# Optimization experiments

Hardware: AMD Instinct MI355X
Metric: run time of the kernel (lower is better)

Reference implementation:

```python
import jax, jax.numpy as jnp
import numpy as np

# dims: B batch, R seq_num (MSA rows), L seq_len (residues), D emb_dim, C n_emb_2D, H heads
B, R, L, D, C, H = 1, 256, 384, 512, 256, 4
HD = D // H
SCALE = np.float32((HD ** -0.5) / np.sqrt(L))  # head-dim scaling * seqlen_scaling (1/sqrt(L))
EPS = 1e-5


def setup_inputs() -> dict:
    key = jax.random.key(0)
    ks = jax.random.split(key, 6)
    s = 0.02
    return {
        "x": jax.random.normal(ks[0], (B, R, L, D), jnp.float32),
        "pair_feat": jax.random.normal(ks[1], (B, L, L, C), jnp.float32),
        "attn_mask": jnp.ones((B, L), jnp.int32),
        "ln_msa_g": jnp.ones((D,), jnp.float32),
        "ln_msa_b": jnp.zeros((D,), jnp.float32),
        "ln_pair_g": jnp.ones((C,), jnp.float32),
        "ln_pair_b": jnp.zeros((C,), jnp.float32),
        "W_pair": jax.random.normal(ks[2], (C, H), jnp.float32) * s,  # stacked per-head [C,1] linears
        "W_v": jax.random.normal(ks[3], (D, D), jnp.float32) * s,     # stacked per-head [D,HD] value proj
        "W_out": jax.random.normal(ks[4], (D, D), jnp.float32) * s,   # to_out (bias=False)
    }


def _ln(x, g, b):
    mu = jnp.mean(x, axis=-1, keepdims=True)
    var = jnp.mean(jnp.square(x - mu), axis=-1, keepdims=True)
    return (x - mu) * jax.lax.rsqrt(var + EPS) * g + b


def reference(x, pair_feat, attn_mask, ln_msa_g, ln_msa_b, ln_pair_g, ln_pair_b, W_pair, W_v, W_out):
    # MHPair_to_MSA.forward (eval mode, dropout=0)
    msa = _ln(x, ln_msa_g, ln_msa_b)                                  # [B,R,L,D]
    pf = (pair_feat + jnp.swapaxes(pair_feat, 1, 2)) * 0.5            # symmetrize
    pf = _ln(pf, ln_pair_g, ln_pair_b)                                # [B,L,L,C]
    # pair-feature-derived attention logits (no QK^T)
    logits = jnp.einsum('bijc,ch->bhij', pf * SCALE, W_pair)          # [B,H,L,L]
    V = jnp.einsum('brld,de->brle', msa, W_v).reshape(B, R, L, H, HD) # [B,R,L,H,HD]
    mask2 = attn_mask[:, :, None] * attn_mask[:, None, :]             # [B,L,L]
    logits = jnp.where(mask2[:, None, :, :] == 0,
                       jnp.finfo(logits.dtype).min, logits)
    attn = jax.nn.softmax(logits, axis=-1)                            # [B,H,L,L]
    out = jnp.einsum('bhij,brjhd->brihd', attn, V).reshape(B, R, L, D)
    out = out @ W_out                                                 # to_out, bias=False
    return x + out                                                    # residual
```

## Files before the change

kernel.cpp:

```cpp
#include <hip/hip_runtime.h>

#define L_   384
#define D_   512
#define C_   256
#define H_   4
#define RR_  256
#define M1_  98304
#define LL2_ 147456
#define NPAIR_BLOCKS 18480

typedef __bf16 bf16x8 __attribute__((ext_vector_type(8)));
typedef float f32x4 __attribute__((ext_vector_type(4)));

__device__ __forceinline__ unsigned short f2bf_bits(float f) {
  union { float f; unsigned u; } v; v.f = f;
  return (unsigned short)((v.u + 0x7fffu + ((v.u >> 16) & 1u)) >> 16);
}
__device__ __forceinline__ __bf16 f2bf(float f) {
  union { unsigned short s; __bf16 b; } o; o.s = f2bf_bits(f);
  return o.b;
}

__global__ __launch_bounds__(256) void ln_msa_kernel(
    const float* __restrict__ x, const float* __restrict__ g,
    const float* __restrict__ b, __bf16* __restrict__ msa) {
  int row = blockIdx.x * 4 + (threadIdx.x >> 6);
  int lane = threadIdx.x & 63;
  const float4* xr = (const float4*)(x + (size_t)row * D_ + lane * 8);
  float4 v0 = xr[0], v1 = xr[1];
  float s1 = v0.x + v0.y + v0.z + v0.w + v1.x + v1.y + v1.z + v1.w;
  float s2 = v0.x * v0.x + v0.y * v0.y + v0.z * v0.z + v0.w * v0.w +
             v1.x * v1.x + v1.y * v1.y + v1.z * v1.z + v1.w * v1.w;
#pragma unroll
  for (int o = 32; o > 0; o >>= 1) {
    s1 += __shfl_xor(s1, o);
    s2 += __shfl_xor(s2, o);
  }
  float mu = s1 * (1.0f / D_);
  float var = s2 * (1.0f / D_) - mu * mu;
  float rs = rsqrtf(var + 1e-5f);
  const float4* gp = (const float4*)(g + lane * 8);
  const float4* bp = (const float4*)(b + lane * 8);
  float4 g0 = gp[0], g1 = gp[1], b0 = bp[0], b1 = bp[1];
  float y[8];
  y[0] = (v0.x - mu) * rs * g0.x + b0.x;
  y[1] = (v0.y - mu) * rs * g0.y + b0.y;
  y[2] = (v0.z - mu) * rs * g0.z + b0.z;
  y[3] = (v0.w - mu) * rs * g0.w + b0.w;
  y[4] = (v1.x - mu) * rs * g1.x + b1.x;
  y[5] = (v1.y - mu) * rs * g1.y + b1.y;
  y[6] = (v1.z - mu) * rs * g1.z + b1.z;
  y[7] = (v1.w - mu) * rs * g1.w + b1.w;
  uint4 pk;
  pk.x = ((unsigned)f2bf_bits(y[1]) << 16) | f2bf_bits(y[0]);
  pk.y = ((unsigned)f2bf_bits(y[3]) << 16) | f2bf_bits(y[2]);
  pk.z = ((unsigned)f2bf_bits(y[5]) << 16) | f2bf_bits(y[4]);
  pk.w = ((unsigned)f2bf_bits(y[7]) << 16) | f2bf_bits(y[6]);
  *(uint4*)(msa + (size_t)row * D_ + lane * 8) = pk;
}

__global__ __launch_bounds__(256) void pair_logits_kernel(
    const float* __restrict__ pf, const int* __restrict__ mask,
    const float* __restrict__ g, const float* __restrict__ b,
    const float* __restrict__ Wp, float* __restrict__ logits) {
  unsigned wid = blockIdx.x * 4 + (threadIdx.x >> 6);
  int lane = threadIdx.x & 63;
  unsigned a = wid / 385u;
  unsigned c = wid - a * 385u;
  int i, j;
  if (c < 384u - a) { i = a; j = a + c; }
  else { i = 383 - a; j = i + (c - (384 - a)); }

  int c0 = lane * 4;
  float4 p1 = *(const float4*)(pf + ((size_t)i * L_ + j) * C_ + c0);
  float4 p2 = *(const float4*)(pf + ((size_t)j * L_ + i) * C_ + c0);
  float4 v;
  v.x = 0.5f * (p1.x + p2.x); v.y = 0.5f * (p1.y + p2.y);
  v.z = 0.5f * (p1.z + p2.z); v.w = 0.5f * (p1.w + p2.w);
  float s1 = v.x + v.y + v.z + v.w;
  float s2 = v.x * v.x + v.y * v.y + v.z * v.z + v.w * v.w;
#pragma unroll
  for (int o = 32; o > 0; o >>= 1) {
    s1 += __shfl_xor(s1, o);
    s2 += __shfl_xor(s2, o);
  }
  float mu = s1 * (1.0f / C_);
  float var = s2 * (1.0f / C_) - mu * mu;
  float rs = rsqrtf(var + 1e-5f);
  float4 gv = *(const float4*)(g + c0);
  float4 bv = *(const float4*)(b + c0);
  float y0 = (v.x - mu) * rs * gv.x + bv.x;
  float y1 = (v.y - mu) * rs * gv.y + bv.y;
  float y2 = (v.z - mu) * rs * gv.z + bv.z;
  float y3 = (v.w - mu) * rs * gv.w + bv.w;
  const float4* wp = (const float4*)Wp;
  float4 w0 = wp[c0], w1 = wp[c0 + 1], w2 = wp[c0 + 2], w3 = wp[c0 + 3];
  float4 t;
  t.x = y0 * w0.x + y1 * w1.x + y2 * w2.x + y3 * w3.x;
  t.y = y0 * w0.y + y1 * w1.y + y2 * w2.y + y3 * w3.y;
  t.z = y0 * w0.z + y1 * w1.z + y2 * w2.z + y3 * w3.z;
  t.w = y0 * w0.w + y1 * w1.w + y2 * w2.w + y3 * w3.w;
#pragma unroll
  for (int o = 32; o > 0; o >>= 1) {
    t.x += __shfl_xor(t.x, o);
    t.y += __shfl_xor(t.y, o);
    t.z += __shfl_xor(t.z, o);
    t.w += __shfl_xor(t.w, o);
  }
  if (lane < 8) {
    int h = lane & 3;
    int ii = (lane < 4) ? i : j;
    int jj = (lane < 4) ? j : i;
    bool ok = (mask[i] != 0) && (mask[j] != 0);
    const float NEG = -3.402823466e38f;
    const float SCALE = (float)(0.08838834764831845 / 19.595917942265423);
    float th = (h == 0) ? t.x : (h == 1) ? t.y : (h == 2) ? t.z : t.w;
    logits[(size_t)h * LL2_ + (size_t)ii * L_ + jj] = ok ? SCALE * th : NEG;
  }
}

__global__ __launch_bounds__(256) void softmax_kernel(
    const float* __restrict__ logits, __bf16* __restrict__ attn) {
  int wave = threadIdx.x >> 6, lane = threadIdx.x & 63;
  int row = blockIdx.x * 4 + wave;
  const float* lr = logits + (size_t)row * L_;
  float v[6];
#pragma unroll
  for (int t = 0; t < 6; ++t) v[t] = lr[lane + t * 64];
  float mx = v[0];
#pragma unroll
  for (int t = 1; t < 6; ++t) mx = fmaxf(mx, v[t]);
#pragma unroll
  for (int o = 32; o > 0; o >>= 1) mx = fmaxf(mx, __shfl_xor(mx, o));
  float s = 0.f;
#pragma unroll
  for (int t = 0; t < 6; ++t) { v[t] = __expf(v[t] - mx); s += v[t]; }
#pragma unroll
  for (int o = 32; o > 0; o >>= 1) s += __shfl_xor(s, o);
  float inv = 1.0f / s;
  __bf16* ar = attn + (size_t)row * L_;
#pragma unroll
  for (int t = 0; t < 6; ++t) ar[lane + t * 64] = f2bf(v[t] * inv);
}

__global__ __launch_bounds__(256) void wtrans_kernel(
    const float* __restrict__ Wv, const float* __restrict__ Wo,
    __bf16* __restrict__ WvT, __bf16* __restrict__ WoT) {
  int id = blockIdx.x * 256 + threadIdx.x;
  int m = id >> 18;
  int e = (id >> 9) & 511, d = id & 511;
  const float* W = m ? Wo : Wv;
  __bf16* T = m ? WoT : WvT;
  T[(size_t)e * 512 + d] = f2bf(W[(size_t)d * 512 + e]);
}

__device__ __forceinline__ void gload16(const void* g, void* l) {
  __builtin_amdgcn_global_load_lds(
      (const __attribute__((address_space(1))) void*)g,
      (__attribute__((address_space(3))) void*)l, 16, 0, 0);
}

__device__ __forceinline__ unsigned xcd_swz_3072(unsigned bid) {
  return (bid & 7u) * 384u + (bid >> 3);
}
__device__ __forceinline__ unsigned xcd_swz_768(unsigned bid) {
  return (bid & 7u) * 96u + (bid >> 3);
}

template <int NT>
__device__ __forceinline__ void stage_part32(__bf16* s, const __bf16* g, size_t ld) {
  int tid = threadIdx.x;
#pragma unroll
  for (int i = 0; i < 2; ++i) {
    int cid = i * NT + tid;
    int row = cid >> 2, c = cid & 3;
    int cs = c ^ ((row >> 1) & 3);
    gload16(g + (size_t)row * ld + cs * 8, (char*)s + cid * 16);
  }
}

__device__ __forceinline__ bf16x8 frag_ld32(const __bf16* s, int row, int fk) {
  int c = (fk >> 3) ^ ((row >> 1) & 3);
  return *(const bf16x8*)((const char*)s + row * 64 + c * 16);
}

__device__ __forceinline__ void mainloop256_2s(
    const __bf16* __restrict__ A, size_t ldA,
    const __bf16* __restrict__ B, size_t ldB,
    int K, __bf16* lds, f32x4 acc[8][4]) {
  int lane = threadIdx.x & 63, wave = threadIdx.x >> 6;
  int wm = (wave >> 2) * 128, wn = (wave & 3) * 64;
  int fr = lane & 15, fk = (lane >> 4) * 8;
  int nt = K >> 5;
  const int SLOT = 512 * 32;
  stage_part32<512>(lds, A, ldA);
  stage_part32<512>(lds + 256 * 32, B, ldB);
  for (int t = 0; t < nt; ++t) {
    const __bf16* As = lds + (t & 1) * SLOT;
    const __bf16* Bs = As + 256 * 32;
    if (t + 1 < nt) {
      __bf16* d = lds + ((t + 1) & 1) * SLOT;
      stage_part32<512>(d, A + (size_t)(t + 1) * 32, ldA);
      stage_part32<512>(d + 256 * 32, B + (size_t)(t + 1) * 32, ldB);
      asm volatile("s_waitcnt vmcnt(4)" ::: "memory");
    } else {
      asm volatile("s_waitcnt vmcnt(0)" ::: "memory");
    }
    __builtin_amdgcn_s_barrier();
    bf16x8 bfv[4];
#pragma unroll
    for (int ni = 0; ni < 4; ++ni) bfv[ni] = frag_ld32(Bs, wn + ni * 16 + fr, fk);
#pragma unroll
    for (int half = 0; half < 2; ++half) {
      bf16x8 af[4];
#pragma unroll
      for (int mi = 0; mi < 4; ++mi)
        af[mi] = frag_ld32(As, wm + half * 64 + mi * 16 + fr, fk);
      __builtin_amdgcn_s_setprio(1);
#pragma unroll
      for (int mi = 0; mi < 4; ++mi)
#pragma unroll
        for (int ni = 0; ni < 4; ++ni)
          acc[half * 4 + mi][ni] = __builtin_amdgcn_mfma_f32_16x16x32_bf16(
              af[mi], bfv[ni], acc[half * 4 + mi][ni], 0, 0, 0);
      __builtin_amdgcn_s_setprio(0);
    }
  }
}

__device__ __forceinline__ void mainloop128(
    const __bf16* __restrict__ A, size_t ldA,
    const __bf16* __restrict__ B, size_t ldB,
    int K, __bf16* lds, f32x4 acc[4][4]) {
  int lane = threadIdx.x & 63, wave = threadIdx.x >> 6;
  int wm = (wave >> 1) * 64, wn = (wave & 1) * 64;
  int fr = lane & 15, fk = (lane >> 4) * 8;
  int nt = K >> 5;
  const int SLOT = 256 * 32;
#pragma unroll
  for (int t = 0; t < 3; ++t) {
    stage_part32<256>(lds + t * SLOT, A + t * 32, ldA);
    stage_part32<256>(lds + t * SLOT + 128 * 32, B + t * 32, ldB);
  }
  for (int t = 0; t < nt; ++t) {
    int rem = nt - 1 - t;
    if (rem >= 2)      asm volatile("s_waitcnt vmcnt(8)" ::: "memory");
    else if (rem == 1) asm volatile("s_waitcnt vmcnt(4)" ::: "memory");
    else               asm volatile("s_waitcnt vmcnt(0)" ::: "memory");
    __builtin_amdgcn_s_barrier();
    const __bf16* As = lds + (t & 3) * SLOT;
    const __bf16* Bs = As + 128 * 32;
    if (t + 3 < nt) {
      __bf16* d = lds + ((t + 3) & 3) * SLOT;
      stage_part32<256>(d, A + (size_t)(t + 3) * 32, ldA);
      stage_part32<256>(d + 128 * 32, B + (size_t)(t + 3) * 32, ldB);
    }
    bf16x8 bfv[4];
#pragma unroll
    for (int ni = 0; ni < 4; ++ni) bfv[ni] = frag_ld32(Bs, wn + ni * 16 + fr, fk);
#pragma unroll
    for (int half = 0; half < 2; ++half) {
      bf16x8 af[2];
#pragma unroll
      for (int mi = 0; mi < 2; ++mi)
        af[mi] = frag_ld32(As, wm + half * 32 + mi * 16 + fr, fk);
      __builtin_amdgcn_s_setprio(1);
#pragma unroll
      for (int mi = 0; mi < 2; ++mi)
#pragma unroll
        for (int ni = 0; ni < 4; ++ni)
          acc[half * 2 + mi][ni] = __builtin_amdgcn_mfma_f32_16x16x32_bf16(
              af[mi], bfv[ni], acc[half * 2 + mi][ni], 0, 0, 0);
      __builtin_amdgcn_s_setprio(0);
    }
  }
}

__global__ __launch_bounds__(512) void gemm_vt_kernel(
    const __bf16* __restrict__ WvT, const __bf16* __restrict__ msa,
    __bf16* __restrict__ VT) {
  __shared__ __bf16 lds[2 * 512 * 32];
  unsigned swz = xcd_swz_768(blockIdx.x + 2 * blockIdx.y);
  int m0 = (swz & 1) * 256;
  int n0 = (swz >> 1) * 256;
  f32x4 acc[8][4] = {};
  mainloop256_2s(WvT + (size_t)m0 * D_, D_, msa + (size_t)n0 * D_, D_, D_, lds, acc);
  int lane = threadIdx.x & 63, wave = threadIdx.x >> 6;
  int wn = (wave & 3) * 64;
  int cr = (lane >> 4) * 4, cc = lane & 15;
  __bf16* Ep = lds;

  __syncthreads();
#pragma unroll
  for (int p = 0; p < 4; ++p) {
    if ((wave >> 2) == (p >> 1)) {
      int mi0 = (p & 1) * 4;
#pragma unroll
      for (int mi = 0; mi < 4; ++mi)
#pragma unroll
        for (int ni = 0; ni < 4; ++ni)
#pragma unroll
          for (int rr = 0; rr < 4; ++rr) {
            int rowl = mi * 16 + cr + rr;
            int col = wn + ni * 16 + cc;
            int cch = col >> 3;
            Ep[rowl * 256 + (((cch ^ (rowl & 31)) << 3) | (col & 7))] =
                f2bf(acc[mi0 + mi][ni][rr]);
          }
    }
    __syncthreads();
#pragma unroll
    for (int s = 0; s < 4; ++s) {
      int rowl = wave * 8 + s * 2 + (lane >> 5);
      int cch = lane & 31;
      bf16x8 v = *(const bf16x8*)&Ep[rowl * 256 + ((cch ^ (rowl & 31)) << 3)];
      int e = m0 + p * 64 + rowl;
      *(bf16x8*)(VT + (size_t)e * M1_ + n0 + cch * 8) = v;
    }
    __syncthreads();
  }
}

__global__ __launch_bounds__(256) void attnv_kernel(
    const __bf16* __restrict__ attn, const __bf16* __restrict__ VT,
    __bf16* __restrict__ out2) {
  __shared__ __bf16 lds[4 * 256 * 32];
  unsigned swz = xcd_swz_3072(blockIdx.x + 3 * blockIdx.y);
  int it = swz % 3u;
  int rh = swz / 3u;
  int h = rh & 3, r = rh >> 2;
  const __bf16* A = attn + (size_t)h * LL2_ + (size_t)it * 128 * L_;
  const __bf16* Bt = VT + (size_t)(h * 128) * M1_ + (size_t)r * L_;
  f32x4 acc[4][4] = {};
  mainloop128(A, L_, Bt, M1_, L_, lds, acc);
  int lane = threadIdx.x & 63, wave = threadIdx.x >> 6;
  int wm = (wave >> 1) * 64, wn = (wave & 1) * 64;
  int cr = (lane >> 4) * 4, cc = lane & 15;
  __bf16* Ep = lds;

  __syncthreads();
#pragma unroll
  for (int mi = 0; mi < 4; ++mi)
#pragma unroll
    for (int ni = 0; ni < 4; ++ni)
#pragma unroll
      for (int rr = 0; rr < 4; ++rr) {
        int il = wm + mi * 16 + cr + rr;
        int el = wn + ni * 16 + cc;
        int cch = el >> 3;
        Ep[il * 128 + (((cch ^ (il & 15)) << 3) | (el & 7))] =
            f2bf(acc[mi][ni][rr]);
      }
  __syncthreads();
#pragma unroll
  for (int s = 0; s < 8; ++s) {
    int il = wave * 32 + s * 4 + (lane >> 4);
    int cch = lane & 15;
    bf16x8 v = *(const bf16x8*)&Ep[il * 128 + ((cch ^ (il & 15)) << 3)];
    *(bf16x8*)(out2 + ((size_t)(r * L_ + it * 128 + il)) * D_ + h * 128 + cch * 8) = v;
  }
}

__global__ __launch_bounds__(512) void gemm_out_kernel(
    const __bf16* __restrict__ out2, const __bf16* __restrict__ WoT,
    const float* __restrict__ x, float* __restrict__ out) {
  __shared__ __bf16 lds[2 * 512 * 32];
  unsigned swz = xcd_swz_768(blockIdx.x + 2 * blockIdx.y);
  int n0 = (swz & 1) * 256;
  int m0 = (swz >> 1) * 256;
  f32x4 acc[8][4] = {};
  mainloop256_2s(out2 + (size_t)m0 * D_, D_, WoT + (size_t)n0 * D_, D_, D_, lds, acc);
  int lane = threadIdx.x & 63, wave = threadIdx.x >> 6;
  int wn = (wave & 3) * 64;
  int cr = (lane >> 4) * 4, cc = lane & 15;
  float* Ep = (float*)lds;

  __syncthreads();
#pragma unroll
  for (int p = 0; p < 4; ++p) {
    if ((wave >> 2) == (p >> 1)) {
      int mi0 = (p & 1) * 4;
#pragma unroll
      for (int mi = 0; mi < 4; ++mi)
#pragma unroll
        for (int ni = 0; ni < 4; ++ni)
#pragma unroll
          for (int rr = 0; rr < 4; ++rr) {
            int rowl = mi * 16 + cr + rr;
            int col = wn + ni * 16 + cc;
            int c4 = col >> 2;
            Ep[rowl * 256 + (((c4 ^ (rowl & 15)) << 2) | (col & 3))] =
                acc[mi0 + mi][ni][rr];
          }
    }
    __syncthreads();
#pragma unroll
    for (int s = 0; s < 8; ++s) {
      int rowl = wave * 8 + s;
      int grow = m0 + p * 64 + rowl;
      float4 v = *(float4*)&Ep[rowl * 256 + ((lane ^ (rowl & 15)) << 2)];
      float4 xv = *(const float4*)(x + (size_t)grow * D_ + n0 + lane * 4);
      v.x += xv.x; v.y += xv.y; v.z += xv.z; v.w += xv.w;
      *(float4*)(out + (size_t)grow * D_ + n0 + lane * 4) = v;
    }
    __syncthreads();
  }
}

extern "C" void kernel_launch(void* const* d_in, const int* in_sizes, int n_in,
                              void* d_out, int out_size, void* d_ws, size_t ws_size,
                              hipStream_t stream) {
  const float* x      = (const float*)d_in[0];
  const float* pair   = (const float*)d_in[1];
  const int*   mask   = (const int*)d_in[2];
  const float* g_msa  = (const float*)d_in[3];
  const float* b_msa  = (const float*)d_in[4];
  const float* g_pair = (const float*)d_in[5];
  const float* b_pair = (const float*)d_in[6];
  const float* Wp     = (const float*)d_in[7];
  const float* Wv     = (const float*)d_in[8];
  const float* Wo     = (const float*)d_in[9];
  float* out = (float*)d_out;

  char* p = (char*)d_ws;
  auto alloc = [&](size_t bytes) {
    char* r = p;
    p += (bytes + 255) & ~(size_t)255;
    return r;
  };
  __bf16* msa    = (__bf16*)alloc((size_t)M1_ * D_ * 2);
  __bf16* VT     = (__bf16*)alloc((size_t)D_ * M1_ * 2);
  float*  logits = (float*)alloc((size_t)H_ * LL2_ * 4);
  __bf16* attn   = (__bf16*)alloc((size_t)H_ * LL2_ * 2);
  __bf16* WvT    = (__bf16*)alloc((size_t)512 * 512 * 2);
  __bf16* WoT    = (__bf16*)alloc((size_t)512 * 512 * 2);
  __bf16* out2   = msa;

  wtrans_kernel<<<2048, 256, 0, stream>>>(Wv, Wo, WvT, WoT);
  ln_msa_kernel<<<M1_ / 4, 256, 0, stream>>>(x, g_msa, b_msa, msa);
  gemm_vt_kernel<<<dim3(2, M1_ / 256), 512, 0, stream>>>(WvT, msa, VT);
  pair_logits_kernel<<<NPAIR_BLOCKS, 256, 0, stream>>>(pair, mask, g_pair, b_pair, Wp, logits);
  softmax_kernel<<<(H_ * L_) / 4, 256, 0, stream>>>(logits, attn);
  attnv_kernel<<<dim3(3, RR_ * H_), 256, 0, stream>>>(attn, VT, out2);
  gemm_out_kernel<<<dim3(2, M1_ / 256), 512, 0, stream>>>(out2, WoT, x, out);
}
```

Measured before the change: 362.9 us.

## Fuse independent kernels into two heterogeneous launches

Merges the LayerNorm of the MSA with the weight transpose into one launch, and the value-projection GEMM with the pair-logit computation into another, dispatching on block index. This removes two kernel launches and lets the memory-bound pair-feature pass overlap with the compute-bound GEMM. Pair blocks now use 512 threads and inherit the GEMM's static shared memory allocation, which may lower their occupancy.

After: 390.6 us. 1.08x slower.

```diff
diff --git a/kernel.cpp b/kernel.cpp
--- a/kernel.cpp
+++ b/kernel.cpp
@@ -7,7 +7,9 @@
 #define RR_  256
 #define M1_  98304
 #define LL2_ 147456
-#define NPAIR_BLOCKS 18480
+#define NVT_BLOCKS 768
+#define NPAIR_FAT 9240
+#define NLN_BLOCKS 24576
 
 typedef __bf16 bf16x8 __attribute__((ext_vector_type(8)));
 typedef float f32x4 __attribute__((ext_vector_type(4)));
@@ -21,101 +23,52 @@
   return o.b;
 }
 
-__global__ __launch_bounds__(256) void ln_msa_kernel(
+__global__ __launch_bounds__(256) void ln_wtrans_kernel(
     const float* __restrict__ x, const float* __restrict__ g,
-    const float* __restrict__ b, __bf16* __restrict__ msa) {
-  int row = blockIdx.x * 4 + (threadIdx.x >> 6);
-  int lane = threadIdx.x & 63;
-  const float4* xr = (const float4*)(x + (size_t)row * D_ + lane * 8);
-  float4 v0 = xr[0], v1 = xr[1];
-  float s1 = v0.x + v0.y + v0.z + v0.w + v1.x + v1.y + v1.z + v1.w;
-  float s2 = v0.x * v0.x + v0.y * v0.y + v0.z * v0.z + v0.w * v0.w +
-             v1.x * v1.x + v1.y * v1.y + v1.z * v1.z + v1.w * v1.w;
-#pragma unroll
-  for (int o = 32; o > 0; o >>= 1) {
-    s1 += __shfl_xor(s1, o);
-    s2 += __shfl_xor(s2, o);
-  }
-  float mu = s1 * (1.0f / D_);
-  float var = s2 * (1.0f / D_) - mu * mu;
-  float rs = rsqrtf(var + 1e-5f);
-  const float4* gp = (const float4*)(g + lane * 8);
-  const float4* bp = (const float4*)(b + lane * 8);
-  float4 g0 = gp[0], g1 = gp[1], b0 = bp[0], b1 = bp[1];
-  float y[8];
-  y[0] = (v0.x - mu) * rs * g0.x + b0.x;
-  y[1] = (v0.y - mu) * rs * g0.y + b0.y;
-  y[2] = (v0.z - mu) * rs * g0.z + b0.z;
-  y[3] = (v0.w - mu) * rs * g0.w + b0.w;
-  y[4] = (v1.x - mu) * rs * g1.x + b1.x;
-  y[5] = (v1.y - mu) * rs * g1.y + b1.y;
-  y[6] = (v1.z - mu) * rs * g1.z + b1.z;
-  y[7] = (v1.w - mu) * rs * g1.w + b1.w;
-  uint4 pk;
-  pk.x = ((unsigned)f2bf_bits(y[1]) << 16) | f2bf_bits(y[0]);
-  pk.y = ((unsigned)f2bf_bits(y[3]) << 16) | f2bf_bits(y[2]);
-  pk.z = ((unsigned)f2bf_bits(y[5]) << 16) | f2bf_bits(y[4]);
-  pk.w = ((unsigned)f2bf_bits(y[7]) << 16) | f2bf_bits(y[6]);
-  *(uint4*)(msa + (size_t)row * D_ + lane * 8) = pk;
-}
-
-__global__ __launch_bounds__(256) void pair_logits_kernel(
-    const float* __restrict__ pf, const int* __restrict__ mask,
-    const float* __restrict__ g, const float* __restrict__ b,
-    const float* __restrict__ Wp, float* __restrict__ logits) {
-  unsigned wid = blockIdx.x * 4 + (threadIdx.x >> 6);
-  int lane = threadIdx.x & 63;
-  unsigned a = wid / 385u;
-  unsigned c = wid - a * 385u;
-  int i, j;
-  if (c < 384u - a) { i = a; j = a + c; }
-  else { i = 383 - a; j = i + (c - (384 - a)); }
-
-  int c0 = lane * 4;
-  float4 p1 = *(const float4*)(pf + ((size_t)i * L_ + j) * C_ + c0);
-  float4 p2 = *(const float4*)(pf + ((size_t)j * L_ + i) * C_ + c0);
-  float4 v;
-  v.x = 0.5f * (p1.x + p2.x); v.y = 0.5f * (p1.y + p2.y);
-  v.z = 0.5f * (p1.z + p2.z); v.w = 0.5f * (p1.w + p2.w);
-  float s1 = v.x + v.y + v.z + v.w;
-  float s2 = v.x * v.x + v.y * v.y + v.z * v.z + v.w * v.w;
-#pragma unroll
-  for (int o = 32; o > 0; o >>= 1) {
-    s1 += __shfl_xor(s1, o);
-    s2 += __shfl_xor(s2, o);
-  }
-  float mu = s1 * (1.0f / C_);
-  float var = s2 * (1.0f / C_) - mu * mu;
-  float rs = rsqrtf(var + 1e-5f);
-  float4 gv = *(const float4*)(g + c0);
-  float4 bv = *(const float4*)(b + c0);
-  float y0 = (v.x - mu) * rs * gv.x + bv.x;
-  float y1 = (v.y - mu) * rs * gv.y + bv.y;
-  float y2 = (v.z - mu) * rs * gv.z + bv.z;
-  float y3 = (v.w - mu) * rs * gv.w + bv.w;
-  const float4* wp = (const float4*)Wp;
-  float4 w0 = wp[c0], w1 = wp[c0 + 1], w2 = wp[c0 + 2], w3 = wp[c0 + 3];
-  float4 t;
-  t.x = y0 * w0.x + y1 * w1.x + y2 * w2.x + y3 * w3.x;
-  t.y = y0 * w0.y + y1 * w1.y + y2 * w2.y + y3 * w3.y;
-  t.z = y0 * w0.z + y1 * w1.z + y2 * w2.z + y3 * w3.z;
-  t.w = y0 * w0.w + y1 * w1.w + y2 * w2.w + y3 * w3.w;
-#pragma unroll
-  for (int o = 32; o > 0; o >>= 1) {
-    t.x += __shfl_xor(t.x, o);
-    t.y += __shfl_xor(t.y, o);
-    t.z += __shfl_xor(t.z, o);
-    t.w += __shfl_xor(t.w, o);
-  }
-  if (lane < 8) {
-    int h = lane & 3;
-    int ii = (lane < 4) ? i : j;
-    int jj = (lane < 4) ? j : i;
-    bool ok = (mask[i] != 0) && (mask[j] != 0);
-    const float NEG = -3.402823466e38f;
-    const float SCALE = (float)(0.08838834764831845 / 19.595917942265423);
-    float th = (h == 0) ? t.x : (h == 1) ? t.y : (h == 2) ? t.z : t.w;
-    logits[(size_t)h * LL2_ + (size_t)ii * L_ + jj] = ok ? SCALE * th : NEG;
+    const float* __restrict__ b, __bf16* __restrict__ msa,
+    const float* __restrict__ Wv, const float* __restrict__ Wo,
+    __bf16* __restrict__ WvT, __bf16* __restrict__ WoT) {
+  if (blockIdx.x < NLN_BLOCKS) {
+    int row = blockIdx.x * 4 + (threadIdx.x >> 6);
+    int lane = threadIdx.x & 63;
+    const float4* xr = (const float4*)(x + (size_t)row * D_ + lane * 8);
+    float4 v0 = xr[0], v1 = xr[1];
+    float s1 = v0.x + v0.y + v0.z + v0.w + v1.x + v1.y + v1.z + v1.w;
+    float s2 = v0.x * v0.x + v0.y * v0.y + v0.z * v0.z + v0.w * v0.w +
+               v1.x * v1.x + v1.y * v1.y + v1.z * v1.z + v1.w * v1.w;
+#pragma unroll
+    for (int o = 32; o > 0; o >>= 1) {
+      s1 += __shfl_xor(s1, o);
+      s2 += __shfl_xor(s2, o);
+    }
+    float mu = s1 * (1.0f / D_);
+    float var = s2 * (1.0f / D_) - mu * mu;
+    float rs = rsqrtf(var + 1e-5f);
+    const float4* gp = (const float4*)(g + lane * 8);
+    const float4* bp = (const float4*)(b + lane * 8);
+    float4 g0 = gp[0], g1 = gp[1], b0 = bp[0], b1 = bp[1];
+    float y[8];
+    y[0] = (v0.x - mu) * rs * g0.x + b0.x;
+    y[1] = (v0.y - mu) * rs * g0.y + b0.y;
+    y[2] = (v0.z - mu) * rs * g0.z + b0.z;
+    y[3] = (v0.w - mu) * rs * g0.w + b0.w;
+    y[4] = (v1.x - mu) * rs * g1.x + b1.x;
+    y[5] = (v1.y - mu) * rs * g1.y + b1.y;
+    y[6] = (v1.z - mu) * rs * g1.z + b1.z;
+    y[7] = (v1.w - mu) * rs * g1.w + b1.w;
+    uint4 pk;
+    pk.x = ((unsigned)f2bf_bits(y[1]) << 16) | f2bf_bits(y[0]);
+    pk.y = ((unsigned)f2bf_bits(y[3]) << 16) | f2bf_bits(y[2]);
+    pk.z = ((unsigned)f2bf_bits(y[5]) << 16) | f2bf_bits(y[4]);
+    pk.w = ((unsigned)f2bf_bits(y[7]) << 16) | f2bf_bits(y[6]);
+    *(uint4*)(msa + (size_t)row * D_ + lane * 8) = pk;
+  } else {
+    int id = (blockIdx.x - NLN_BLOCKS) * 256 + threadIdx.x;
+    int m = id >> 18;
+    int e = (id >> 9) & 511, d = id & 511;
+    const float* W = m ? Wo : Wv;
+    __bf16* T = m ? WoT : WvT;
+    T[(size_t)e * 512 + d] = f2bf(W[(size_t)d * 512 + e]);
   }
 }
 
@@ -141,17 +94,6 @@
   __bf16* ar = attn + (size_t)row * L_;
 #pragma unroll
   for (int t = 0; t < 6; ++t) ar[lane + t * 64] = f2bf(v[t] * inv);
-}
-
-__global__ __launch_bounds__(256) void wtrans_kernel(
-    const float* __restrict__ Wv, const float* __restrict__ Wo,
-    __bf16* __restrict__ WvT, __bf16* __restrict__ WoT) {
-  int id = blockIdx.x * 256 + threadIdx.x;
-  int m = id >> 18;
-  int e = (id >> 9) & 511, d = id & 511;
-  const float* W = m ? Wo : Wv;
-  __bf16* T = m ? WoT : WvT;
-  T[(size_t)e * 512 + d] = f2bf(W[(size_t)d * 512 + e]);
 }
 
 __device__ __forceinline__ void gload16(const void* g, void* l) {
@@ -276,48 +218,108 @@
   }
 }
 
-__global__ __launch_bounds__(512) void gemm_vt_kernel(
+__global__ __launch_bounds__(512) void vt_pair_kernel(
     const __bf16* __restrict__ WvT, const __bf16* __restrict__ msa,
-    __bf16* __restrict__ VT) {
+    __bf16* __restrict__ VT,
+    const float* __restrict__ pf, const int* __restrict__ mask,
+    const float* __restrict__ gp_, const float* __restrict__ bp_,
+    const float* __restrict__ Wp, float* __restrict__ logits) {
   __shared__ __bf16 lds[2 * 512 * 32];
-  unsigned swz = xcd_swz_768(blockIdx.x + 2 * blockIdx.y);
-  int m0 = (swz & 1) * 256;
-  int n0 = (swz >> 1) * 256;
-  f32x4 acc[8][4] = {};
-  mainloop256_2s(WvT + (size_t)m0 * D_, D_, msa + (size_t)n0 * D_, D_, D_, lds, acc);
-  int lane = threadIdx.x & 63, wave = threadIdx.x >> 6;
-  int wn = (wave & 3) * 64;
-  int cr = (lane >> 4) * 4, cc = lane & 15;
-  __bf16* Ep = lds;
-
-  __syncthreads();
-#pragma unroll
-  for (int p = 0; p < 4; ++p) {
-    if ((wave >> 2) == (p >> 1)) {
-      int mi0 = (p & 1) * 4;
-#pragma unroll
-      for (int mi = 0; mi < 4; ++mi)
-#pragma unroll
-        for (int ni = 0; ni < 4; ++ni)
-#pragma unroll
-          for (int rr = 0; rr < 4; ++rr) {
-            int rowl = mi * 16 + cr + rr;
-            int col = wn + ni * 16 + cc;
-            int cch = col >> 3;
-            Ep[rowl * 256 + (((cch ^ (rowl & 31)) << 3) | (col & 7))] =
-                f2bf(acc[mi0 + mi][ni][rr]);
-          }
-    }
+  if (blockIdx.x < NVT_BLOCKS) {
+    unsigned swz = xcd_swz_768(blockIdx.x);
+    int m0 = (swz & 1) * 256;
+    int n0 = (swz >> 1) * 256;
+    f32x4 acc[8][4] = {};
+    mainloop256_2s(WvT + (size_t)m0 * D_, D_, msa + (size_t)n0 * D_, D_, D_, lds, acc);
+    int lane = threadIdx.x & 63, wave = threadIdx.x >> 6;
+    int wn = (wave & 3) * 64;
+    int cr = (lane >> 4) * 4, cc = lane & 15;
+    __bf16* Ep = lds;
+
     __syncthreads();
 #pragma unroll
-    for (int s = 0; s < 4; ++s) {
-      int rowl = wave * 8 + s * 2 + (lane >> 5);
-      int cch = lane & 31;
-      bf16x8 v = *(const bf16x8*)&Ep[rowl * 256 + ((cch ^ (rowl & 31)) << 3)];
-      int e = m0 + p * 64 + rowl;
-      *(bf16x8*)(VT + (size_t)e * M1_ + n0 + cch * 8) = v;
-    }
-    __syncthreads();
+    for (int p = 0; p < 4; ++p) {
+      if ((wave >> 2) == (p >> 1)) {
+        int mi0 = (p & 1) * 4;
+#pragma unroll
+        for (int mi = 0; mi < 4; ++mi)
+#pragma unroll
+          for (int ni = 0; ni < 4; ++ni)
+#pragma unroll
+            for (int rr = 0; rr < 4; ++rr) {
+              int rowl = mi * 16 + cr + rr;
+              int col = wn + ni * 16 + cc;
+              int cch = col >> 3;
+              Ep[rowl * 256 + (((cch ^ (rowl & 31)) << 3) | (col & 7))] =
+                  f2bf(acc[mi0 + mi][ni][rr]);
+            }
+      }
+      __syncthreads();
+#pragma unroll
+      for (int s = 0; s < 4; ++s) {
+        int rowl = wave * 8 + s * 2 + (lane >> 5);
+        int cch = lane & 31;
+        bf16x8 v = *(const bf16x8*)&Ep[rowl * 256 + ((cch ^ (rowl & 31)) << 3)];
+        int e = m0 + p * 64 + rowl;
+        *(bf16x8*)(VT + (size_t)e * M1_ + n0 + cch * 8) = v;
+      }
+      __syncthreads();
+    }
+  } else {
+    int wave = threadIdx.x >> 6, lane = threadIdx.x & 63;
+    unsigned wid = (blockIdx.x - NVT_BLOCKS) * 8 + wave;
+    unsigned a = wid / 385u;
+    unsigned c = wid - a * 385u;
+    int i, j;
+    if (c < 384u - a) { i = a; j = a + c; }
+    else { i = 383 - a; j = i + (c - (384 - a)); }
+
+    int c0 = lane * 4;
+    float4 p1 = *(const float4*)(pf + ((size_t)i * L_ + j) * C_ + c0);
+    float4 p2 = *(const float4*)(pf + ((size_t)j * L_ + i) * C_ + c0);
+    float4 v;
+    v.x = 0.5f * (p1.x + p2.x); v.y = 0.5f * (p1.y + p2.y);
+    v.z = 0.5f * (p1.z + p2.z); v.w = 0.5f * (p1.w + p2.w);
+    float s1 = v.x + v.y + v.z + v.w;
+    float s2 = v.x * v.x + v.y * v.y + v.z * v.z + v.w * v.w;
+#pragma unroll
+    for (int o = 32; o > 0; o >>= 1) {
+      s1 += __shfl_xor(s1, o);
+      s2 += __shfl_xor(s2, o);
+    }
+    float mu = s1 * (1.0f / C_);
+    float var = s2 * (1.0f / C_) - mu * mu;
+    float rs = rsqrtf(var + 1e-5f);
+    float4 gv = *(const float4*)(gp_ + c0);
+    float4 bv = *(const float4*)(bp_ + c0);
+    float y0 = (v.x - mu) * rs * gv.x + bv.x;
+    float y1 = (v.y - mu) * rs * gv.y + bv.y;
+    float y2 = (v.z - mu) * rs * gv.z + bv.z;
+    float y3 = (v.w - mu) * rs * gv.w + bv.w;
+    const float4* wp = (const float4*)Wp;
+    float4 w0 = wp[c0], w1 = wp[c0 + 1], w2 = wp[c0 + 2], w3 = wp[c0 + 3];
+    float4 t;
+    t.x = y0 * w0.x + y1 * w1.x + y2 * w2.x + y3 * w3.x;
+    t.y = y0 * w0.y + y1 * w1.y + y2 * w2.y + y3 * w3.y;
+    t.z = y0 * w0.z + y1 * w1.z + y2 * w2.z + y3 * w3.z;
+    t.w = y0 * w0.w + y1 * w1.w + y2 * w2.w + y3 * w3.w;
+#pragma unroll
+    for (int o = 32; o > 0; o >>= 1) {
+      t.x += __shfl_xor(t.x, o);
+      t.y += __shfl_xor(t.y, o);
+      t.z += __shfl_xor(t.z, o);
+      t.w += __shfl_xor(t.w, o);
+    }
+    if (lane < 8) {
+      int h = lane & 3;
+      int ii = (lane < 4) ? i : j;
+      int jj = (lane < 4) ? j : i;
+      bool ok = (mask[i] != 0) && (mask[j] != 0);
+      const float NEG = -3.402823466e38f;
+      const float SCALE = (float)(0.08838834764831845 / 19.595917942265423);
+      float th = (h == 0) ? t.x : (h == 1) ? t.y : (h == 2) ? t.z : t.w;
+      logits[(size_t)h * LL2_ + (size_t)ii * L_ + jj] = ok ? SCALE * th : NEG;
+    }
   }
 }
 
@@ -436,10 +438,10 @@
   __bf16* WoT    = (__bf16*)alloc((size_t)512 * 512 * 2);
   __bf16* out2   = msa;
 
-  wtrans_kernel<<<2048, 256, 0, stream>>>(Wv, Wo, WvT, WoT);
-  ln_msa_kernel<<<M1_ / 4, 256, 0, stream>>>(x, g_msa, b_msa, msa);
-  gemm_vt_kernel<<<dim3(2, M1_ / 256), 512, 0, stream>>>(WvT, msa, VT);
-  pair_logits_kernel<<<NPAIR_BLOCKS, 256, 0, stream>>>(pair, mask, g_pair, b_pair, Wp, logits);
+  ln_wtrans_kernel<<<NLN_BLOCKS + 2048, 256, 0, stream>>>(
+      x, g_msa, b_msa, msa, Wv, Wo, WvT, WoT);
+  vt_pair_kernel<<<NVT_BLOCKS + NPAIR_FAT, 512, 0, stream>>>(
+      WvT, msa, VT, pair, mask, g_pair, b_pair, Wp, logits);
   softmax_kernel<<<(H_ * L_) / 4, 256, 0, stream>>>(logits, attn);
   attnv_kernel<<<dim3(3, RR_ * H_), 256, 0, stream>>>(attn, VT, out2);
   gemm_out_kernel<<<dim3(2, M1_ / 256), 512, 0, stream>>>(out2, WoT, x, out);
```
